# Kernel tuning notes

Hardware: AMD Instinct MI355X
Metric: run time of the kernel (lower is better)

The kernel has to match this reference:

```python
import jax, jax.numpy as jnp
import numpy as np

V, E_DIM, H, B, T = 390, 256, 512, 64, 512
START = 388


def setup_inputs() -> dict:
    key = jax.random.key(0)
    ks = jax.random.split(key, 32)
    s = 0.05
    rn = lambda k, shape: jax.random.normal(k, shape, jnp.float32) * s
    inp = {
        "input": jax.random.normal(ks[0], (B, T, V), jnp.float32),
        # encoder params
        "enc_emb": rn(ks[1], (V, E_DIM)),
        "enc_Wih0": rn(ks[2], (3 * H, E_DIM)),
        "enc_Whh0": rn(ks[3], (3 * H, H)),
        "enc_bih0": rn(ks[4], (3 * H,)),
        "enc_bhh0": rn(ks[5], (3 * H,)),
        "enc_Wih1": rn(ks[6], (3 * H, H)),
        "enc_Whh1": rn(ks[7], (3 * H, H)),
        "enc_bih1": rn(ks[8], (3 * H,)),
        "enc_bhh1": rn(ks[9], (3 * H,)),
        # decoder params
        "dec_emb": rn(ks[10], (V, E_DIM)),
        "dec_Wih0": rn(ks[11], (3 * H, E_DIM)),
        "dec_Whh0": rn(ks[12], (3 * H, H)),
        "dec_bih0": rn(ks[13], (3 * H,)),
        "dec_bhh0": rn(ks[14], (3 * H,)),
        "dec_Wih1": rn(ks[15], (3 * H, H)),
        "dec_Whh1": rn(ks[16], (3 * H, H)),
        "dec_bih1": rn(ks[17], (3 * H,)),
        "dec_bhh1": rn(ks[18], (3 * H,)),
        # prediction head
        "Wp1": rn(ks[19], (H, H)),
        "bp1": rn(ks[20], (H,)),
        "Wp2": rn(ks[21], (V, H)),
        "bp2": rn(ks[22], (V,)),
    }
    return inp


def _gru_cell(x, h, Wih, Whh, bih, bhh):
    # PyTorch GRU cell: gates ordered (r, z, n)
    gi = x @ Wih.T + bih
    gh = h @ Whh.T + bhh
    ir, iz, inn = jnp.split(gi, 3, axis=-1)
    hr, hz, hn = jnp.split(gh, 3, axis=-1)
    r = jax.nn.sigmoid(ir + hr)
    z = jax.nn.sigmoid(iz + hz)
    n = jnp.tanh(inn + r * hn)
    return (1.0 - z) * n + z * h


def reference(input, enc_emb, enc_Wih0, enc_Whh0, enc_bih0, enc_bhh0,
              enc_Wih1, enc_Whh1, enc_bih1, enc_bhh1,
              dec_emb, dec_Wih0, dec_Whh0, dec_bih0, dec_bhh0,
              dec_Wih1, dec_Whh1, dec_bih1, dec_bhh1,
              Wp1, bp1, Wp2, bp2):
    batch, max_len, vocab = input.shape
    hdim = enc_Whh0.shape[1]

    # ---- Encoder: soft embedding + 2-layer GRU, keep final hidden states ----
    x = jnp.einsum('btv,ve->bte', input, enc_emb)  # [B,T,E]
    xt = jnp.transpose(x, (1, 0, 2))               # time-major [T,B,E]
    h0 = jnp.zeros((batch, hdim), input.dtype)

    def step0(h, xt_):
        h = _gru_cell(xt_, h, enc_Wih0, enc_Whh0, enc_bih0, enc_bhh0)
        return h, h
    h1_enc, seq1 = jax.lax.scan(step0, h0, xt)

    def step1(h, xt_):
        h = _gru_cell(xt_, h, enc_Wih1, enc_Whh1, enc_bih1, enc_bhh1)
        return h, None
    h2_enc, _ = jax.lax.scan(step1, h0, seq1)

    tok0 = jnp.full((batch,), START, jnp.int32)
    rng0 = jax.random.key(42)

    def dec_step(carry, _):
        h1, h2, tok, rng = carry
        rng, sk = jax.random.split(rng)
        xe = dec_emb[tok]                               # [B,E]
        h1 = _gru_cell(xe, h1, dec_Wih0, dec_Whh0, dec_bih0, dec_bhh0)
        h2 = _gru_cell(h1, h2, dec_Wih1, dec_Whh1, dec_bih1, dec_bhh1)
        hid = h2 @ Wp1.T + bp1
        hid = jnp.where(hid >= 0, hid, 0.1 * hid)       # LeakyReLU(0.1)
        logits = hid @ Wp2.T + bp2                      # temp=1 -> logits/temp == logits
        probs = jax.nn.softmax(logits, axis=-1)
        tok = jax.random.categorical(sk, logits, axis=-1).astype(jnp.int32)
        return (h1, h2, tok, rng), (probs, tok)

    _, (probs_seq, toks) = jax.lax.scan(
        dec_step, (h1_enc, h2_enc, tok0, rng0), None, length=max_len - 1)

    start_oh = jax.nn.one_hot(tok0, vocab, dtype=input.dtype)  # [B,V]
    outputs = jnp.concatenate(
        [start_oh[:, None, :], jnp.transpose(probs_seq, (1, 0, 2))], axis=1)
    max_output = jnp.concatenate(
        [jnp.full((batch, 1), float(START), jnp.float32),
         toks.T.astype(jnp.float32)], axis=1)
    return outputs, max_output
```

## Files before the change

### kernel.cpp

```cpp
#include <hip/hip_runtime.h>
#include <math.h>


#define BB 64
#define TT 512
#define VV 390
#define EE 256
#define HH 512

#define SW(k, b) ((((k) >> 2) << 8) + ((b) << 2) + ((k) & 3))

static __device__ __forceinline__ void tf2x32(unsigned k0, unsigned k1,
                                              unsigned x0, unsigned x1,
                                              unsigned &o0, unsigned &o1) {
  unsigned ks2 = k0 ^ k1 ^ 0x1BD11BDAu;
  x0 += k0; x1 += k1;
#define TFR(r) x0 += x1; x1 = (x1 << (r)) | (x1 >> (32 - (r))); x1 ^= x0;
  TFR(13) TFR(15) TFR(26) TFR(6)
  x0 += k1; x1 += ks2 + 1u;
  TFR(17) TFR(29) TFR(16) TFR(24)
  x0 += ks2; x1 += k0 + 2u;
  TFR(13) TFR(15) TFR(26) TFR(6)
  x0 += k0; x1 += k1 + 3u;
  TFR(17) TFR(29) TFR(16) TFR(24)
  x0 += k1; x1 += ks2 + 4u;
  TFR(13) TFR(15) TFR(26) TFR(6)
  x0 += ks2; x1 += k0 + 5u;
#undef TFR
  o0 = x0; o1 = x1;
}

static __device__ __forceinline__ float sigm(float x) {
  return 1.0f / (1.0f + expf(-x));
}

static __device__ __forceinline__ unsigned ldu_a(const unsigned* p) {
  return __hip_atomic_load((unsigned*)p, __ATOMIC_RELAXED,
                           __HIP_MEMORY_SCOPE_AGENT);
}
static __device__ __forceinline__ void stu_a(unsigned* p, unsigned v) {
  __hip_atomic_store(p, v, __ATOMIC_RELAXED, __HIP_MEMORY_SCOPE_AGENT);
}
static __device__ __forceinline__ float ldf_a(const float* p) {
  return __uint_as_float(ldu_a((const unsigned*)p));
}
static __device__ __forceinline__ void stf_a(float* p, float v) {
  stu_a((unsigned*)p, __float_as_uint(v));
}
static __device__ __forceinline__ float2 ldf2_a(const float* p) {
  unsigned long long v = __hip_atomic_load((unsigned long long*)p,
      __ATOMIC_RELAXED, __HIP_MEMORY_SCOPE_AGENT);
  return make_float2(__uint_as_float((unsigned)v),
                     __uint_as_float((unsigned)(v >> 32)));
}

template <int K>
static __device__ __forceinline__ void dot3s_a(const float* __restrict__ X, int b,
    const float* __restrict__ w0, const float* __restrict__ w1,
    const float* __restrict__ w2, float &r0, float &r1, float &r2) {
  const float4* q0 = (const float4*)w0;
  const float4* q1 = (const float4*)w1;
  const float4* q2 = (const float4*)w2;
  const float* Xb = X + (b << 2);
  float s0 = 0.f, s1 = 0.f, s2 = 0.f;
#pragma unroll
  for (int k4 = 0; k4 < (K >> 2); ++k4) {
    float2 xa = ldf2_a(Xb + (k4 << 8));
    float2 xc = ldf2_a(Xb + (k4 << 8) + 2);
    float4 u0 = q0[k4], u1 = q1[k4], u2 = q2[k4];
    s0 = fmaf(xa.x, u0.x, s0); s0 = fmaf(xa.y, u0.y, s0); s0 = fmaf(xc.x, u0.z, s0); s0 = fmaf(xc.y, u0.w, s0);
    s1 = fmaf(xa.x, u1.x, s1); s1 = fmaf(xa.y, u1.y, s1); s1 = fmaf(xc.x, u1.z, s1); s1 = fmaf(xc.y, u1.w, s1);
    s2 = fmaf(xa.x, u2.x, s2); s2 = fmaf(xa.y, u2.y, s2); s2 = fmaf(xc.x, u2.z, s2); s2 = fmaf(xc.y, u2.w, s2);
  }
  r0 = s0; r1 = s1; r2 = s2;
}

template <int K>
static __device__ __forceinline__ float dot1s_a(const float* __restrict__ X, int b,
    const float* __restrict__ w) {
  const float4* q = (const float4*)w;
  const float* Xb = X + (b << 2);
  float s = 0.f;
#pragma unroll
  for (int k4 = 0; k4 < (K >> 2); ++k4) {
    float2 xa = ldf2_a(Xb + (k4 << 8));
    float2 xc = ldf2_a(Xb + (k4 << 8) + 2);
    float4 u = q[k4];
    s = fmaf(xa.x, u.x, s); s = fmaf(xa.y, u.y, s);
    s = fmaf(xc.x, u.z, s); s = fmaf(xc.y, u.w, s);
  }
  return s;
}

template <int K>
static __device__ __forceinline__ void dot3s_p(const float* __restrict__ X, int b,
    const float* __restrict__ w0, const float* __restrict__ w1,
    const float* __restrict__ w2, float &r0, float &r1, float &r2) {
  const float4* q0 = (const float4*)w0;
  const float4* q1 = (const float4*)w1;
  const float4* q2 = (const float4*)w2;
  const float4* Xp = (const float4*)X;
  float s0 = 0.f, s1 = 0.f, s2 = 0.f;
#pragma unroll
  for (int k4 = 0; k4 < (K >> 2); ++k4) {
    float4 x = Xp[(k4 << 6) + b];
    float4 u0 = q0[k4], u1 = q1[k4], u2 = q2[k4];
    s0 = fmaf(x.x, u0.x, s0); s0 = fmaf(x.y, u0.y, s0); s0 = fmaf(x.z, u0.z, s0); s0 = fmaf(x.w, u0.w, s0);
    s1 = fmaf(x.x, u1.x, s1); s1 = fmaf(x.y, u1.y, s1); s1 = fmaf(x.z, u1.z, s1); s1 = fmaf(x.w, u1.w, s1);
    s2 = fmaf(x.x, u2.x, s2); s2 = fmaf(x.y, u2.y, s2); s2 = fmaf(x.z, u2.z, s2); s2 = fmaf(x.w, u2.w, s2);
  }
  r0 = s0; r1 = s1; r2 = s2;
}

template <int K>
static __device__ __forceinline__ void dot3_row(const float* __restrict__ xrow,
    const float* __restrict__ w0, const float* __restrict__ w1,
    const float* __restrict__ w2, float &r0, float &r1, float &r2) {
  const float4* xq = (const float4*)xrow;
  const float4* q0 = (const float4*)w0;
  const float4* q1 = (const float4*)w1;
  const float4* q2 = (const float4*)w2;
  float s0 = 0.f, s1 = 0.f, s2 = 0.f;
#pragma unroll
  for (int k4 = 0; k4 < (K >> 2); ++k4) {
    float4 x = xq[k4];
    float4 u0 = q0[k4], u1 = q1[k4], u2 = q2[k4];
    s0 = fmaf(x.x, u0.x, s0); s0 = fmaf(x.y, u0.y, s0); s0 = fmaf(x.z, u0.z, s0); s0 = fmaf(x.w, u0.w, s0);
    s1 = fmaf(x.x, u1.x, s1); s1 = fmaf(x.y, u1.y, s1); s1 = fmaf(x.z, u1.z, s1); s1 = fmaf(x.w, u1.w, s1);
    s2 = fmaf(x.x, u2.x, s2); s2 = fmaf(x.y, u2.y, s2); s2 = fmaf(x.z, u2.z, s2); s2 = fmaf(x.w, u2.w, s2);
  }
  r0 = s0; r1 = s1; r2 = s2;
}

template <int NWG>
static __device__ __forceinline__ void bar(unsigned* flags, int wg, unsigned ep) {
  __syncthreads();
  int tid = threadIdx.x;
  if (tid == 0) stu_a(flags + wg, ep);
  if (tid < 64) {
    bool ok;
    do {
      ok = true;
#pragma unroll
      for (int i = 0; i < NWG; i += 64)
        ok &= (ldu_a(flags + i + tid) >= ep);
    } while (!__all(ok));
  }
  __syncthreads();
}

__global__ __launch_bounds__(256) void k_init(float* out,
    float* h1buf, float* h2buf, int* tok, unsigned* ebase) {
  int wg = blockIdx.x, tid = threadIdx.x;
  for (int i = wg * 256 + tid; i < HH * BB; i += 64 * 256) {
    h1buf[i] = 0.f;
    h2buf[i] = 0.f;
  }
  for (int v = tid; v < VV; v += 256)
    out[(size_t)wg * TT * VV + v] = (v == 388) ? 1.0f : 0.0f;
  if (wg == 0) {
    ebase[tid] = 0u;
    ebase[tid + 256] = 0u;
  }
  if (tid == 0) {
    out[(size_t)BB * TT * VV + (size_t)wg * TT] = 388.0f;
    tok[wg] = 388;
  }
}

__global__ __launch_bounds__(256) void k_xgemm(const float* __restrict__ input,
    const float* __restrict__ emb, float* __restrict__ xT) {
  int t = blockIdx.x, tid = threadIdx.x;
  int s = tid >> 6, b = tid & 63;
  __shared__ float lin[64 * 65];
  float4 acc[16];
#pragma unroll
  for (int i = 0; i < 16; ++i) acc[i] = make_float4(0.f, 0.f, 0.f, 0.f);
  for (int k0 = 0; k0 < VV; k0 += 64) {
    int kmax = min(64, VV - k0);
    __syncthreads();
#pragma unroll
    for (int r = 0; r < 16; ++r) {
      int idx = r * 256 + tid;
      int b2 = idx >> 6, kk = idx & 63;
      if (kk < kmax)
        lin[kk * 65 + b2] = input[((size_t)b2 * TT + t) * VV + k0 + kk];
    }
    __syncthreads();
    for (int kk = 0; kk < kmax; ++kk) {
      float xv = lin[kk * 65 + b];
      const float4* er = (const float4*)(emb + (size_t)(k0 + kk) * EE);
#pragma unroll
      for (int i = 0; i < 16; ++i) {
        float4 w = er[s + 4 * i];
        acc[i].x = fmaf(xv, w.x, acc[i].x);
        acc[i].y = fmaf(xv, w.y, acc[i].y);
        acc[i].z = fmaf(xv, w.z, acc[i].z);
        acc[i].w = fmaf(xv, w.w, acc[i].w);
      }
    }
  }
  float* dst0 = xT + (size_t)t * (EE * 64);
#pragma unroll
  for (int i = 0; i < 16; ++i) {
    *(float4*)(dst0 + (s + 4 * i) * 256 + 4 * b) = acc[i];
  }
}

__global__ __launch_bounds__(256, 2) void k_enc(
    const float* __restrict__ xT, float* h1buf, float* h2buf,
    const float* __restrict__ Wih0, const float* __restrict__ Whh0,
    const float* __restrict__ bih0, const float* __restrict__ bhh0,
    const float* __restrict__ Wih1, const float* __restrict__ Whh1,
    const float* __restrict__ bih1, const float* __restrict__ bhh1,
    unsigned* eflags, unsigned* dbase) {
  int wg = blockIdx.x, tid = threadIdx.x;
  int s = tid >> 6, b = tid & 63;
  int cs = s & 1, task = s >> 1;
  bool lay1 = (wg >= 256);
  int j = (lay1 ? (wg - 256) : wg) * 2 + cs;
  __shared__ float part[2][3][64];
  for (int t = 0; t <= TT; ++t) {
    const float* h1_r = h1buf + (t & 1) * (HH * BB);
    float* h1_w = h1buf + ((t + 1) & 1) * (HH * BB);
    bool active = lay1 ? (t >= 1) : (t < TT);
    float ar = 0.f, az = 0.f, an = 0.f;
    if (active) {
      if (!lay1) {
        if (task == 0) {
          dot3s_p<EE>(xT + (size_t)t * (EE * 64), b,
                      Wih0 + (size_t)j * EE, Wih0 + (size_t)(512 + j) * EE,
                      Wih0 + (size_t)(1024 + j) * EE, ar, az, an);
        } else {
          float hr, hz, hn;
          dot3s_a<HH>(h1_r, b,
                      Whh0 + (size_t)j * HH, Whh0 + (size_t)(512 + j) * HH,
                      Whh0 + (size_t)(1024 + j) * HH, hr, hz, hn);
          part[cs][0][b] = hr; part[cs][1][b] = hz; part[cs][2][b] = hn;
        }
      } else {
        if (task == 0) {
          dot3s_a<HH>(h1_r, b,
                      Wih1 + (size_t)j * HH, Wih1 + (size_t)(512 + j) * HH,
                      Wih1 + (size_t)(1024 + j) * HH, ar, az, an);
        } else {
          const float* h2_r = h2buf + ((t + 1) & 1) * (HH * BB);
          float hr, hz, hn;
          dot3s_a<HH>(h2_r, b,
                      Whh1 + (size_t)j * HH, Whh1 + (size_t)(512 + j) * HH,
                      Whh1 + (size_t)(1024 + j) * HH, hr, hz, hn);
          part[cs][0][b] = hr; part[cs][1][b] = hz; part[cs][2][b] = hn;
        }
      }
    }
    __syncthreads();
    if (active && task == 0) {
      float hr = part[cs][0][b], hz = part[cs][1][b], hn = part[cs][2][b];
      if (!lay1) {
        float r = sigm((ar + bih0[j]) + (hr + bhh0[j]));
        float z = sigm((az + bih0[512 + j]) + (hz + bhh0[512 + j]));
        float n = tanhf((an + bih0[1024 + j]) + r * (hn + bhh0[1024 + j]));
        float hp = ldf_a(h1_r + SW(j, b));
        stf_a(h1_w + SW(j, b), (1.0f - z) * n + z * hp);
      } else {
        const float* h2_r = h2buf + ((t + 1) & 1) * (HH * BB);
        float* h2_w = h2buf + (t & 1) * (HH * BB);
        float r = sigm((ar + bih1[j]) + (hr + bhh1[j]));
        float z = sigm((az + bih1[512 + j]) + (hz + bhh1[512 + j]));
        float n = tanhf((an + bih1[1024 + j]) + r * (hn + bhh1[1024 + j]));
        float hp = ldf_a(h2_r + SW(j, b));
        stf_a(h2_w + SW(j, b), (1.0f - z) * n + z * hp);
      }
    }
    if (t == 2 && wg == 0 && tid < 64) {
#pragma unroll
      for (int i = 0; i < 256; i += 64) stu_a(dbase + i + tid, 0u);
    }
    if (t < TT) bar<512>(eflags, wg, (unsigned)(t + 1));
  }
}

__global__ __launch_bounds__(256) void k_dec(
    float* h1buf, float* h2buf,
    const float* __restrict__ demb,
    const float* __restrict__ dWih0, const float* __restrict__ dWhh0,
    const float* __restrict__ dbih0, const float* __restrict__ dbhh0,
    const float* __restrict__ dWih1, const float* __restrict__ dWhh1,
    const float* __restrict__ dbih1, const float* __restrict__ dbhh1,
    const float* __restrict__ Wp1, const float* __restrict__ bp1,
    const float* __restrict__ Wp2, const float* __restrict__ bp2,
    float* out, int* tok, unsigned* dflags, float* hid) {
  int wg = blockIdx.x, tid = threadIdx.x;
  int s = tid >> 6, b = tid & 63;
  int cs = s & 1, task = s >> 1;
  int j = wg * 2 + cs;
  __shared__ float part[2][3][64];
  __shared__ __align__(16) float lhid[HH];
  __shared__ float rf[8];
  __shared__ int ri[4];
  unsigned rk0 = 0u, rk1 = 42u;
  unsigned ep = 0u;
  for (int d = 0; d < TT - 1; ++d) {
    const float* h1_r = h1buf + (d & 1) * (HH * BB);
    float* h1_w = h1buf + ((d + 1) & 1) * (HH * BB);
    const float* h2_r = h2buf + (d & 1) * (HH * BB);
    float* h2_w = h2buf + ((d + 1) & 1) * (HH * BB);
    {
      float ar = 0.f, az = 0.f, an = 0.f;
      if (task == 1) {
        float hr, hz, hn;
        dot3s_a<HH>(h1_r, b,
                    dWhh0 + (size_t)j * HH, dWhh0 + (size_t)(512 + j) * HH,
                    dWhh0 + (size_t)(1024 + j) * HH, hr, hz, hn);
        part[cs][0][b] = hr; part[cs][1][b] = hz; part[cs][2][b] = hn;
      } else {
        int tk = (int)ldu_a((const unsigned*)tok + b);
        dot3_row<EE>(demb + (size_t)tk * EE,
                     dWih0 + (size_t)j * EE, dWih0 + (size_t)(512 + j) * EE,
                     dWih0 + (size_t)(1024 + j) * EE, ar, az, an);
      }
      __syncthreads();
      if (task == 0) {
        float hr = part[cs][0][b], hz = part[cs][1][b], hn = part[cs][2][b];
        float r = sigm((ar + dbih0[j]) + (hr + dbhh0[j]));
        float z = sigm((az + dbih0[512 + j]) + (hz + dbhh0[512 + j]));
        float n = tanhf((an + dbih0[1024 + j]) + r * (hn + dbhh0[1024 + j]));
        float hp = ldf_a(h1_r + SW(j, b));
        stf_a(h1_w + SW(j, b), (1.0f - z) * n + z * hp);
      }
    }
    bar<256>(dflags, wg, ++ep);
    {
      float ar = 0.f, az = 0.f, an = 0.f;
      if (task == 1) {
        float hr, hz, hn;
        dot3s_a<HH>(h2_r, b,
                    dWhh1 + (size_t)j * HH, dWhh1 + (size_t)(512 + j) * HH,
                    dWhh1 + (size_t)(1024 + j) * HH, hr, hz, hn);
        part[cs][0][b] = hr; part[cs][1][b] = hz; part[cs][2][b] = hn;
      } else {
        dot3s_a<HH>(h1_w, b,
                    dWih1 + (size_t)j * HH, dWih1 + (size_t)(512 + j) * HH,
                    dWih1 + (size_t)(1024 + j) * HH, ar, az, an);
      }
      __syncthreads();
      if (task == 0) {
        float hr = part[cs][0][b], hz = part[cs][1][b], hn = part[cs][2][b];
        float r = sigm((ar + dbih1[j]) + (hr + dbhh1[j]));
        float z = sigm((az + dbih1[512 + j]) + (hz + dbhh1[512 + j]));
        float n = tanhf((an + dbih1[1024 + j]) + r * (hn + dbhh1[1024 + j]));
        float hp = ldf_a(h2_r + SW(j, b));
        stf_a(h2_w + SW(j, b), (1.0f - z) * n + z * hp);
      }
    }
    bar<256>(dflags, wg, ++ep);
    if (task == 0) {
      float a = dot1s_a<HH>(h2_w, b, Wp1 + (size_t)j * HH);
      a += bp1[j];
      stf_a(hid + SW(j, b), (a >= 0.f) ? a : 0.1f * a);
    }
    bar<256>(dflags, wg, ++ep);
    if (wg < BB) {
      int brow = wg;
      if (tid < 128) {
        float2 ha = ldf2_a(hid + tid * 256 + brow * 4);
        float2 hb = ldf2_a(hid + tid * 256 + brow * 4 + 2);
        lhid[4 * tid] = ha.x; lhid[4 * tid + 1] = ha.y;
        lhid[4 * tid + 2] = hb.x; lhid[4 * tid + 3] = hb.y;
      }
      __syncthreads();
      float v0 = 0.f, v1 = 0.f;
      if (tid < VV) {
        const float4* w = (const float4*)(Wp2 + (size_t)tid * HH);
        float a = 0.f;
#pragma unroll 8
        for (int k4 = 0; k4 < HH / 4; ++k4) {
          float4 q = w[k4];
          float4 hv = *(const float4*)&lhid[k4 * 4];
          a = fmaf(hv.x, q.x, a); a = fmaf(hv.y, q.y, a);
          a = fmaf(hv.z, q.z, a); a = fmaf(hv.w, q.w, a);
        }
        v0 = a + bp2[tid];
      }
      if (tid + 256 < VV) {
        const float4* w = (const float4*)(Wp2 + (size_t)(tid + 256) * HH);
        float a = 0.f;
#pragma unroll 8
        for (int k4 = 0; k4 < HH / 4; ++k4) {
          float4 q = w[k4];
          float4 hv = *(const float4*)&lhid[k4 * 4];
          a = fmaf(hv.x, q.x, a); a = fmaf(hv.y, q.y, a);
          a = fmaf(hv.z, q.z, a); a = fmaf(hv.w, q.w, a);
        }
        v1 = a + bp2[tid + 256];
      }
      float m = -INFINITY;
      if (tid < VV) m = fmaxf(m, v0);
      if (tid + 256 < VV) m = fmaxf(m, v1);
      for (int off = 32; off > 0; off >>= 1) m = fmaxf(m, __shfl_down(m, off, 64));
      if ((tid & 63) == 0) rf[tid >> 6] = m;
      __syncthreads();
      if (tid == 0) rf[4] = fmaxf(fmaxf(rf[0], rf[1]), fmaxf(rf[2], rf[3]));
      __syncthreads();
      m = rf[4];
      unsigned sk0, sk1;
      tf2x32(rk0, rk1, 0u, 1u, sk0, sk1);
      float by = -INFINITY; int bc = 0x7fffffff;
      if (tid < VV) {
        unsigned o0, o1;
        tf2x32(sk0, sk1, 0u, (unsigned)(brow * VV + tid), o0, o1);
        unsigned bits = o0 ^ o1;
        float f = __uint_as_float(0x3f800000u | (bits >> 9)) - 1.0f;
        float u = (f > 0.f) ? f : 1.17549435e-38f;
        float g = (float)(-log(-log((double)u)));
        float y = v0 + g;
        if (y > by || (y == by && tid < bc)) { by = y; bc = tid; }
      }
      if (tid + 256 < VV) {
        int c = tid + 256;
        unsigned o0, o1;
        tf2x32(sk0, sk1, 0u, (unsigned)(brow * VV + c), o0, o1);
        unsigned bits = o0 ^ o1;
        float f = __uint_as_float(0x3f800000u | (bits >> 9)) - 1.0f;
        float u = (f > 0.f) ? f : 1.17549435e-38f;
        float g = (float)(-log(-log((double)u)));
        float y = v1 + g;
        if (y > by || (y == by && c < bc)) { by = y; bc = c; }
      }
      for (int off = 32; off > 0; off >>= 1) {
        float oy = __shfl_down(by, off, 64);
        int oc = __shfl_down(bc, off, 64);
        if (oy > by || (oy == by && oc < bc)) { by = oy; bc = oc; }
      }
      if ((tid & 63) == 0) { rf[tid >> 6] = by; ri[tid >> 6] = bc; }
      __syncthreads();
      if (tid == 0) {
        by = rf[0]; bc = ri[0];
        for (int w2 = 1; w2 < 4; ++w2)
          if (rf[w2] > by || (rf[w2] == by && ri[w2] < bc)) { by = rf[w2]; bc = ri[w2]; }
        stu_a((unsigned*)tok + brow, (unsigned)bc);
        out[(size_t)BB * TT * VV + (size_t)brow * TT + (d + 1)] = (float)bc;
      }
      __syncthreads();
      float e0 = 0.f, e1 = 0.f, ssum = 0.f;
      if (tid < VV) { e0 = expf(v0 - m); ssum += e0; }
      if (tid + 256 < VV) { e1 = expf(v1 - m); ssum += e1; }
      for (int off = 32; off > 0; off >>= 1) ssum += __shfl_down(ssum, off, 64);
      if ((tid & 63) == 0) rf[tid >> 6] = ssum;
      __syncthreads();
      if (tid == 0) rf[4] = (rf[0] + rf[1]) + (rf[2] + rf[3]);
      __syncthreads();
      float S = rf[4];
      float* orow = out + ((size_t)brow * TT + (d + 1)) * VV;
      if (tid < VV) orow[tid] = e0 / S;
      if (tid + 256 < VV) orow[tid + 256] = e1 / S;
    }
    {
      unsigned n0, n1;
      tf2x32(rk0, rk1, 0u, 0u, n0, n1);
      rk0 = n0; rk1 = n1;
    }
    if (d < TT - 2) bar<256>(dflags, wg, ++ep);
  }
}

extern "C" void kernel_launch(void* const* d_in, const int* in_sizes, int n_in,
                              void* d_out, int out_size, void* d_ws, size_t ws_size,
                              hipStream_t stream) {
  (void)in_sizes; (void)n_in; (void)out_size; (void)ws_size;
  const float* input = (const float*)d_in[0];
  const float* e_emb = (const float*)d_in[1];
  const float* eWih0 = (const float*)d_in[2];
  const float* eWhh0 = (const float*)d_in[3];
  const float* ebih0 = (const float*)d_in[4];
  const float* ebhh0 = (const float*)d_in[5];
  const float* eWih1 = (const float*)d_in[6];
  const float* eWhh1 = (const float*)d_in[7];
  const float* ebih1 = (const float*)d_in[8];
  const float* ebhh1 = (const float*)d_in[9];
  const float* d_emb = (const float*)d_in[10];
  const float* dWih0 = (const float*)d_in[11];
  const float* dWhh0 = (const float*)d_in[12];
  const float* dbih0 = (const float*)d_in[13];
  const float* dbhh0 = (const float*)d_in[14];
  const float* dWih1 = (const float*)d_in[15];
  const float* dWhh1 = (const float*)d_in[16];
  const float* dbih1 = (const float*)d_in[17];
  const float* dbhh1 = (const float*)d_in[18];
  const float* Wp1   = (const float*)d_in[19];
  const float* bp1   = (const float*)d_in[20];
  const float* Wp2   = (const float*)d_in[21];
  const float* bp2   = (const float*)d_in[22];
  float* out = (float*)d_out;

  float* xT = (float*)d_ws;
  float* h1buf = xT + (size_t)TT * EE * 64;
  float* h2buf = h1buf + 2 * HH * BB;
  int* tok = (int*)(h2buf + 2 * HH * BB);
  unsigned* ebase = (unsigned*)(out + ((size_t)1 * TT + 1) * VV);
  unsigned* dflags = (unsigned*)xT;
  float* hid = xT + 4096;

  k_init<<<64, 256, 0, stream>>>(out, h1buf, h2buf, tok, ebase);
  k_xgemm<<<TT, 256, 0, stream>>>(input, e_emb, xT);
  k_enc<<<512, 256, 0, stream>>>(xT, h1buf, h2buf,
      eWih0, eWhh0, ebih0, ebhh0, eWih1, eWhh1, ebih1, ebhh1, ebase, dflags);
  k_dec<<<256, 256, 0, stream>>>(h1buf, h2buf, d_emb,
      dWih0, dWhh0, dbih0, dbhh0, dWih1, dWhh1, dbih1, dbhh1,
      Wp1, bp1, Wp2, bp2, out, tok, dflags, hid);
}
```

Before: 74.88 ms.

## Partition recurrent work by batch groups with LDS-staged hidden state and group barriers

Workgroups are regrouped so each one handles 16 hidden units times 8 batch rows instead of 2 units times all 64 rows. Each workgroup stages its batch slice of the hidden state into LDS once per step, and the dot products read it from there instead of doing repeated atomic global loads. The grid-wide barriers become per-batch-group barriers (64 or 32 workgroups), which cuts synchronisation fan-in. The cost is that each workgroup now reads 16 weight rows per batch slice, so weight traffic across the grid increases, and more LDS is used per block.

```diff
diff --git a/kernel.cpp b/kernel.cpp
--- a/kernel.cpp
+++ b/kernel.cpp
@@ -54,40 +54,50 @@
                      __uint_as_float((unsigned)(v >> 32)));
 }
 
+static __device__ __forceinline__ void stage512(const float* X, int b0,
+                                                float2* L) {
+  int tid = threadIdx.x;
+  float2 v[8];
+#pragma unroll
+  for (int r = 0; r < 8; ++r) {
+    int i = tid + (r << 8);
+    v[r] = ldf2_a(X + ((i >> 4) << 8) + ((b0 + ((i >> 1) & 7)) << 2) +
+                  ((i & 1) << 1));
+  }
+#pragma unroll
+  for (int r = 0; r < 8; ++r) L[tid + (r << 8)] = v[r];
+}
+
 template <int K>
-static __device__ __forceinline__ void dot3s_a(const float* __restrict__ X, int b,
+static __device__ __forceinline__ void dot3_lds(const float4* Lx, int bi,
     const float* __restrict__ w0, const float* __restrict__ w1,
     const float* __restrict__ w2, float &r0, float &r1, float &r2) {
   const float4* q0 = (const float4*)w0;
   const float4* q1 = (const float4*)w1;
   const float4* q2 = (const float4*)w2;
-  const float* Xb = X + (b << 2);
   float s0 = 0.f, s1 = 0.f, s2 = 0.f;
 #pragma unroll
   for (int k4 = 0; k4 < (K >> 2); ++k4) {
-    float2 xa = ldf2_a(Xb + (k4 << 8));
-    float2 xc = ldf2_a(Xb + (k4 << 8) + 2);
+    float4 x = Lx[(k4 << 3) + bi];
     float4 u0 = q0[k4], u1 = q1[k4], u2 = q2[k4];
-    s0 = fmaf(xa.x, u0.x, s0); s0 = fmaf(xa.y, u0.y, s0); s0 = fmaf(xc.x, u0.z, s0); s0 = fmaf(xc.y, u0.w, s0);
-    s1 = fmaf(xa.x, u1.x, s1); s1 = fmaf(xa.y, u1.y, s1); s1 = fmaf(xc.x, u1.z, s1); s1 = fmaf(xc.y, u1.w, s1);
-    s2 = fmaf(xa.x, u2.x, s2); s2 = fmaf(xa.y, u2.y, s2); s2 = fmaf(xc.x, u2.z, s2); s2 = fmaf(xc.y, u2.w, s2);
+    s0 = fmaf(x.x, u0.x, s0); s0 = fmaf(x.y, u0.y, s0); s0 = fmaf(x.z, u0.z, s0); s0 = fmaf(x.w, u0.w, s0);
+    s1 = fmaf(x.x, u1.x, s1); s1 = fmaf(x.y, u1.y, s1); s1 = fmaf(x.z, u1.z, s1); s1 = fmaf(x.w, u1.w, s1);
+    s2 = fmaf(x.x, u2.x, s2); s2 = fmaf(x.y, u2.y, s2); s2 = fmaf(x.z, u2.z, s2); s2 = fmaf(x.w, u2.w, s2);
   }
   r0 = s0; r1 = s1; r2 = s2;
 }
 
 template <int K>
-static __device__ __forceinline__ float dot1s_a(const float* __restrict__ X, int b,
+static __device__ __forceinline__ float dot1_lds(const float4* Lx, int bi,
     const float* __restrict__ w) {
   const float4* q = (const float4*)w;
-  const float* Xb = X + (b << 2);
   float s = 0.f;
 #pragma unroll
   for (int k4 = 0; k4 < (K >> 2); ++k4) {
-    float2 xa = ldf2_a(Xb + (k4 << 8));
-    float2 xc = ldf2_a(Xb + (k4 << 8) + 2);
+    float4 x = Lx[(k4 << 3) + bi];
     float4 u = q[k4];
-    s = fmaf(xa.x, u.x, s); s = fmaf(xa.y, u.y, s);
-    s = fmaf(xc.x, u.z, s); s = fmaf(xc.y, u.w, s);
+    s = fmaf(x.x, u.x, s); s = fmaf(x.y, u.y, s);
+    s = fmaf(x.z, u.z, s); s = fmaf(x.w, u.w, s);
   }
   return s;
 }
@@ -132,19 +142,17 @@
   r0 = s0; r1 = s1; r2 = s2;
 }
 
-template <int NWG>
-static __device__ __forceinline__ void bar(unsigned* flags, int wg, unsigned ep) {
+static __device__ __forceinline__ void gbar(unsigned* f, int nwg, int wgi,
+                                            unsigned ep) {
   __syncthreads();
   int tid = threadIdx.x;
-  if (tid == 0) stu_a(flags + wg, ep);
+  if (tid == 0) stu_a(f + wgi, ep);
   if (tid < 64) {
     bool ok;
     do {
       ok = true;
-#pragma unroll
-      for (int i = 0; i < NWG; i += 64)
-        ok &= (ldu_a(flags + i + tid) >= ep);
-    } while (!__all(ok));
+      for (int i = tid; i < nwg; i += 64) ok &= (ldu_a(f + i) >= ep);
+    } while (!__all((int)ok));
   }
   __syncthreads();
 }
@@ -202,85 +210,93 @@
   }
   float* dst0 = xT + (size_t)t * (EE * 64);
 #pragma unroll
-  for (int i = 0; i < 16; ++i) {
+  for (int i = 0; i < 16; ++i)
     *(float4*)(dst0 + (s + 4 * i) * 256 + 4 * b) = acc[i];
-  }
 }
 
 __global__ __launch_bounds__(256, 2) void k_enc(
-    const float* __restrict__ xT, float* h1buf, float* h2buf,
+    const float* xT, float* h1buf, float* h2buf,
     const float* __restrict__ Wih0, const float* __restrict__ Whh0,
     const float* __restrict__ bih0, const float* __restrict__ bhh0,
     const float* __restrict__ Wih1, const float* __restrict__ Whh1,
     const float* __restrict__ bih1, const float* __restrict__ bhh1,
-    unsigned* eflags, unsigned* dbase) {
+    unsigned* eflags, unsigned* dflags) {
   int wg = blockIdx.x, tid = threadIdx.x;
-  int s = tid >> 6, b = tid & 63;
-  int cs = s & 1, task = s >> 1;
-  bool lay1 = (wg >= 256);
-  int j = (lay1 ? (wg - 256) : wg) * 2 + cs;
-  __shared__ float part[2][3][64];
+  int g = wg >> 6, wgi = wg & 63;
+  int b0 = g << 3;
+  int lay = wgi >> 5, j0 = (wgi & 31) << 4;
+  int task = tid >> 7, l = tid & 127;
+  int jj = l >> 3, bi = l & 7;
+  int j = j0 + jj, b = b0 + bi;
+  __shared__ float2 sX[2048];
+  __shared__ float2 sY[2048];
+  __shared__ float part[3][128];
+  unsigned* gf = eflags + (g << 6);
   for (int t = 0; t <= TT; ++t) {
     const float* h1_r = h1buf + (t & 1) * (HH * BB);
     float* h1_w = h1buf + ((t + 1) & 1) * (HH * BB);
-    bool active = lay1 ? (t >= 1) : (t < TT);
-    float ar = 0.f, az = 0.f, an = 0.f;
-    if (active) {
-      if (!lay1) {
+    if (lay == 0) {
+      if (t < TT) {
+        stage512(h1_r, b0, sX);
+        __syncthreads();
+        float ar = 0.f, az = 0.f, an = 0.f;
         if (task == 0) {
           dot3s_p<EE>(xT + (size_t)t * (EE * 64), b,
                       Wih0 + (size_t)j * EE, Wih0 + (size_t)(512 + j) * EE,
                       Wih0 + (size_t)(1024 + j) * EE, ar, az, an);
         } else {
           float hr, hz, hn;
-          dot3s_a<HH>(h1_r, b,
-                      Whh0 + (size_t)j * HH, Whh0 + (size_t)(512 + j) * HH,
-                      Whh0 + (size_t)(1024 + j) * HH, hr, hz, hn);
-          part[cs][0][b] = hr; part[cs][1][b] = hz; part[cs][2][b] = hn;
+          dot3_lds<HH>((const float4*)sX, bi,
+                       Whh0 + (size_t)j * HH, Whh0 + (size_t)(512 + j) * HH,
+                       Whh0 + (size_t)(1024 + j) * HH, hr, hz, hn);
+          part[0][l] = hr; part[1][l] = hz; part[2][l] = hn;
         }
-      } else {
+        __syncthreads();
         if (task == 0) {
-          dot3s_a<HH>(h1_r, b,
-                      Wih1 + (size_t)j * HH, Wih1 + (size_t)(512 + j) * HH,
-                      Wih1 + (size_t)(1024 + j) * HH, ar, az, an);
-        } else {
-          const float* h2_r = h2buf + ((t + 1) & 1) * (HH * BB);
-          float hr, hz, hn;
-          dot3s_a<HH>(h2_r, b,
-                      Whh1 + (size_t)j * HH, Whh1 + (size_t)(512 + j) * HH,
-                      Whh1 + (size_t)(1024 + j) * HH, hr, hz, hn);
-          part[cs][0][b] = hr; part[cs][1][b] = hz; part[cs][2][b] = hn;
+          float hr = part[0][l], hz = part[1][l], hn = part[2][l];
+          float r = sigm((ar + bih0[j]) + (hr + bhh0[j]));
+          float z = sigm((az + bih0[512 + j]) + (hz + bhh0[512 + j]));
+          float n = tanhf((an + bih0[1024 + j]) + r * (hn + bhh0[1024 + j]));
+          float hp = ((const float*)sX)[((j >> 2) << 5) + (bi << 2) + (j & 3)];
+          stf_a(h1_w + SW(j, b), (1.0f - z) * n + z * hp);
         }
       }
-    }
-    __syncthreads();
-    if (active && task == 0) {
-      float hr = part[cs][0][b], hz = part[cs][1][b], hn = part[cs][2][b];
-      if (!lay1) {
-        float r = sigm((ar + bih0[j]) + (hr + bhh0[j]));
-        float z = sigm((az + bih0[512 + j]) + (hz + bhh0[512 + j]));
-        float n = tanhf((an + bih0[1024 + j]) + r * (hn + bhh0[1024 + j]));
-        float hp = ldf_a(h1_r + SW(j, b));
-        stf_a(h1_w + SW(j, b), (1.0f - z) * n + z * hp);
-      } else {
+    } else {
+      if (t >= 1) {
         const float* h2_r = h2buf + ((t + 1) & 1) * (HH * BB);
         float* h2_w = h2buf + (t & 1) * (HH * BB);
-        float r = sigm((ar + bih1[j]) + (hr + bhh1[j]));
-        float z = sigm((az + bih1[512 + j]) + (hz + bhh1[512 + j]));
-        float n = tanhf((an + bih1[1024 + j]) + r * (hn + bhh1[1024 + j]));
-        float hp = ldf_a(h2_r + SW(j, b));
-        stf_a(h2_w + SW(j, b), (1.0f - z) * n + z * hp);
-      }
-    }
-    if (t == 2 && wg == 0 && tid < 64) {
-#pragma unroll
-      for (int i = 0; i < 256; i += 64) stu_a(dbase + i + tid, 0u);
-    }
-    if (t < TT) bar<512>(eflags, wg, (unsigned)(t + 1));
-  }
-}
-
-__global__ __launch_bounds__(256) void k_dec(
+        stage512(h1_r, b0, sX);
+        stage512(h2_r, b0, sY);
+        __syncthreads();
+        float ar = 0.f, az = 0.f, an = 0.f;
+        if (task == 0) {
+          dot3_lds<HH>((const float4*)sX, bi,
+                       Wih1 + (size_t)j * HH, Wih1 + (size_t)(512 + j) * HH,
+                       Wih1 + (size_t)(1024 + j) * HH, ar, az, an);
+        } else {
+          float hr, hz, hn;
+          dot3_lds<HH>((const float4*)sY, bi,
+                       Whh1 + (size_t)j * HH, Whh1 + (size_t)(512 + j) * HH,
+                       Whh1 + (size_t)(1024 + j) * HH, hr, hz, hn);
+          part[0][l] = hr; part[1][l] = hz; part[2][l] = hn;
+        }
+        __syncthreads();
+        if (task == 0) {
+          float hr = part[0][l], hz = part[1][l], hn = part[2][l];
+          float r = sigm((ar + bih1[j]) + (hr + bhh1[j]));
+          float z = sigm((az + bih1[512 + j]) + (hz + bhh1[512 + j]));
+          float n = tanhf((an + bih1[1024 + j]) + r * (hn + bhh1[1024 + j]));
+          float hp = ((const float*)sY)[((j >> 2) << 5) + (bi << 2) + (j & 3)];
+          stf_a(h2_w + SW(j, b), (1.0f - z) * n + z * hp);
+        }
+      }
+    }
+    if (t == 2 && wgi == 0 && tid < 32) stu_a(dflags + (g << 5) + tid, 0u);
+    if (t < TT) gbar(gf, 64, wgi, (unsigned)(t + 1));
+  }
+}
+
+__global__ __launch_bounds__(256, 1) void k_dec(
     float* h1buf, float* h2buf,
     const float* __restrict__ demb,
     const float* __restrict__ dWih0, const float* __restrict__ dWhh0,
@@ -291,13 +307,18 @@
     const float* __restrict__ Wp2, const float* __restrict__ bp2,
     float* out, int* tok, unsigned* dflags, float* hid) {
   int wg = blockIdx.x, tid = threadIdx.x;
-  int s = tid >> 6, b = tid & 63;
-  int cs = s & 1, task = s >> 1;
-  int j = wg * 2 + cs;
-  __shared__ float part[2][3][64];
+  int g = wg >> 5, wgi = wg & 31;
+  int b0 = g << 3, j0 = wgi << 4;
+  int task = tid >> 7, l = tid & 127;
+  int jj = l >> 3, bi = l & 7;
+  int j = j0 + jj, b = b0 + bi;
+  __shared__ float2 sX[2048];
+  __shared__ float2 sY[2048];
+  __shared__ float part[3][128];
   __shared__ __align__(16) float lhid[HH];
   __shared__ float rf[8];
   __shared__ int ri[4];
+  unsigned* gf = dflags + (g << 5);
   unsigned rk0 = 0u, rk1 = 42u;
   unsigned ep = 0u;
   for (int d = 0; d < TT - 1; ++d) {
@@ -306,13 +327,15 @@
     const float* h2_r = h2buf + (d & 1) * (HH * BB);
     float* h2_w = h2buf + ((d + 1) & 1) * (HH * BB);
     {
+      stage512(h1_r, b0, sX);
+      __syncthreads();
       float ar = 0.f, az = 0.f, an = 0.f;
       if (task == 1) {
         float hr, hz, hn;
-        dot3s_a<HH>(h1_r, b,
-                    dWhh0 + (size_t)j * HH, dWhh0 + (size_t)(512 + j) * HH,
-                    dWhh0 + (size_t)(1024 + j) * HH, hr, hz, hn);
-        part[cs][0][b] = hr; part[cs][1][b] = hz; part[cs][2][b] = hn;
+        dot3_lds<HH>((const float4*)sX, bi,
+                     dWhh0 + (size_t)j * HH, dWhh0 + (size_t)(512 + j) * HH,
+                     dWhh0 + (size_t)(1024 + j) * HH, hr, hz, hn);
+        part[0][l] = hr; part[1][l] = hz; part[2][l] = hn;
       } else {
         int tk = (int)ldu_a((const unsigned*)tok + b);
         dot3_row<EE>(demb + (size_t)tk * EE,
@@ -321,47 +344,54 @@
       }
       __syncthreads();
       if (task == 0) {
-        float hr = part[cs][0][b], hz = part[cs][1][b], hn = part[cs][2][b];
+        float hr = part[0][l], hz = part[1][l], hn = part[2][l];
         float r = sigm((ar + dbih0[j]) + (hr + dbhh0[j]));
         float z = sigm((az + dbih0[512 + j]) + (hz + dbhh0[512 + j]));
         float n = tanhf((an + dbih0[1024 + j]) + r * (hn + dbhh0[1024 + j]));
-        float hp = ldf_a(h1_r + SW(j, b));
+        float hp = ((const float*)sX)[((j >> 2) << 5) + (bi << 2) + (j & 3)];
         stf_a(h1_w + SW(j, b), (1.0f - z) * n + z * hp);
       }
     }
-    bar<256>(dflags, wg, ++ep);
+    gbar(gf, 32, wgi, ++ep);
     {
+      stage512(h1_w, b0, sX);
+      stage512(h2_r, b0, sY);
+      __syncthreads();
       float ar = 0.f, az = 0.f, an = 0.f;
-      if (task == 1) {
+      if (task == 0) {
+        dot3_lds<HH>((const float4*)sX, bi,
+                     dWih1 + (size_t)j * HH, dWih1 + (size_t)(512 + j) * HH,
+                     dWih1 + (size_t)(1024 + j) * HH, ar, az, an);
+      } else {
         float hr, hz, hn;
-        dot3s_a<HH>(h2_r, b,
-                    dWhh1 + (size_t)j * HH, dWhh1 + (size_t)(512 + j) * HH,
-                    dWhh1 + (size_t)(1024 + j) * HH, hr, hz, hn);
-        part[cs][0][b] = hr; part[cs][1][b] = hz; part[cs][2][b] = hn;
-      } else {
-        dot3s_a<HH>(h1_w, b,
-                    dWih1 + (size_t)j * HH, dWih1 + (size_t)(512 + j) * HH,
-                    dWih1 + (size_t)(1024 + j) * HH, ar, az, an);
+        dot3_lds<HH>((const float4*)sY, bi,
+                     dWhh1 + (size_t)j * HH, dWhh1 + (size_t)(512 + j) * HH,
+                     dWhh1 + (size_t)(1024 + j) * HH, hr, hz, hn);
+        part[0][l] = hr; part[1][l] = hz; part[2][l] = hn;
       }
       __syncthreads();
       if (task == 0) {
-        float hr = part[cs][0][b], hz = part[cs][1][b], hn = part[cs][2][b];
+        float hr = part[0][l], hz = part[1][l], hn = part[2][l];
         float r = sigm((ar + dbih1[j]) + (hr + dbhh1[j]));
         float z = sigm((az + dbih1[512 + j]) + (hz + dbhh1[512 + j]));
         float n = tanhf((an + dbih1[1024 + j]) + r * (hn + dbhh1[1024 + j]));
-        float hp = ldf_a(h2_r + SW(j, b));
+        float hp = ((const float*)sY)[((j >> 2) << 5) + (bi << 2) + (j & 3)];
         stf_a(h2_w + SW(j, b), (1.0f - z) * n + z * hp);
       }
     }
-    bar<256>(dflags, wg, ++ep);
-    if (task == 0) {
-      float a = dot1s_a<HH>(h2_w, b, Wp1 + (size_t)j * HH);
-      a += bp1[j];
-      stf_a(hid + SW(j, b), (a >= 0.f) ? a : 0.1f * a);
-    }
-    bar<256>(dflags, wg, ++ep);
-    if (wg < BB) {
-      int brow = wg;
+    gbar(gf, 32, wgi, ++ep);
+    {
+      stage512(h2_w, b0, sX);
+      __syncthreads();
+      if (tid < 128) {
+        float a = dot1_lds<HH>((const float4*)sX, bi, Wp1 + (size_t)j * HH);
+        a += bp1[j];
+        stf_a(hid + SW(j, b), (a >= 0.f) ? a : 0.1f * a);
+      }
+    }
+    gbar(gf, 32, wgi, ++ep);
+    if (wgi < 8) {
+      int brow = b0 + wgi;
       if (tid < 128) {
         float2 ha = ldf2_a(hid + tid * 256 + brow * 4);
         float2 hb = ldf2_a(hid + tid * 256 + brow * 4 + 2);
@@ -412,8 +442,8 @@
         unsigned bits = o0 ^ o1;
         float f = __uint_as_float(0x3f800000u | (bits >> 9)) - 1.0f;
         float u = (f > 0.f) ? f : 1.17549435e-38f;
-        float g = (float)(-log(-log((double)u)));
-        float y = v0 + g;
+        float gg = (float)(-log(-log((double)u)));
+        float y = v0 + gg;
         if (y > by || (y == by && tid < bc)) { by = y; bc = tid; }
       }
       if (tid + 256 < VV) {
@@ -423,8 +453,8 @@
         unsigned bits = o0 ^ o1;
         float f = __uint_as_float(0x3f800000u | (bits >> 9)) - 1.0f;
         float u = (f > 0.f) ? f : 1.17549435e-38f;
-        float g = (float)(-log(-log((double)u)));
-        float y = v1 + g;
+        float gg = (float)(-log(-log((double)u)));
+        float y = v1 + gg;
         if (y > by || (y == by && c < bc)) { by = y; bc = c; }
       }
       for (int off = 32; off > 0; off >>= 1) {
@@ -460,7 +490,7 @@
       tf2x32(rk0, rk1, 0u, 0u, n0, n1);
       rk0 = n0; rk1 = n1;
     }
-    if (d < TT - 2) bar<256>(dflags, wg, ++ep);
+    if (d < TT - 2) gbar(gf, 32, wgi, ++ep);
   }
 }
 
@@ -497,14 +527,14 @@
   float* h1buf = xT + (size_t)TT * EE * 64;
   float* h2buf = h1buf + 2 * HH * BB;
   int* tok = (int*)(h2buf + 2 * HH * BB);
-  unsigned* ebase = (unsigned*)(out + ((size_t)1 * TT + 1) * VV);
+  unsigned* eflags = (unsigned*)(out + ((size_t)1 * TT + 1) * VV);
   unsigned* dflags = (unsigned*)xT;
   float* hid = xT + 4096;
 
-  k_init<<<64, 256, 0, stream>>>(out, h1buf, h2buf, tok, ebase);
+  k_init<<<64, 256, 0, stream>>>(out, h1buf, h2buf, tok, eflags);
   k_xgemm<<<TT, 256, 0, stream>>>(input, e_emb, xT);
   k_enc<<<512, 256, 0, stream>>>(xT, h1buf, h2buf,
-      eWih0, eWhh0, ebih0, ebhh0, eWih1, eWhh1, ebih1, ebhh1, ebase, dflags);
+      eWih0, eWhh0, ebih0, ebhh0, eWih1, eWhh1, ebih1, ebhh1, eflags, dflags);
   k_dec<<<256, 256, 0, stream>>>(h1buf, h2buf, d_emb,
       dWih0, dWhh0, dbih0, dbhh0, dWih1, dWhh1, dbih1, dbhh1,
       Wp1, bp1, Wp2, bp2, out, tok, dflags, hid);
```

Measured after the change: 73.42 ms. About the same (-2.0%).
